# Kernel tuning notes

Hardware: AMD Instinct MI355X
Metric: run time of the kernel (lower is better)

## Reference

```python
import jax, jax.numpy as jnp
import numpy as np

N_EMBED = 8192
EMBED_DIM = 32
BETA = 0.25
EPS_NORM = 1e-12   # torch F.normalize eps
EPS_ENT = 1e-4     # get_entropy eps


def _l2norm(x):
    n = jnp.linalg.norm(x, axis=-1, keepdims=True)
    return x / jnp.maximum(n, EPS_NORM)


def setup_inputs() -> dict:
    key = jax.random.key(0)
    k1, k2 = jax.random.split(key)
    z = jax.random.normal(k1, (32, EMBED_DIM, 32, 32), dtype=jnp.float32)
    # embedding.weight.data.uniform_(-1/n_embed, 1/n_embed)
    embedding = jax.random.uniform(k2, (N_EMBED, EMBED_DIM), dtype=jnp.float32,
                                   minval=-1.0 / N_EMBED, maxval=1.0 / N_EMBED)
    return {"z": z, "embedding": embedding}


def reference(z, embedding):
    batch = z.shape[0]
    # bchw -> bhwc
    zt = jnp.transpose(z, (0, 2, 3, 1))
    # l2_norm branch: cosine distance via negative inner product
    zn = _l2norm(zt)
    z_flat = zn.reshape(-1, EMBED_DIM)            # [N, D], N = B*H*W
    ew = _l2norm(embedding)                       # [K, D]
    d = -jnp.matmul(z_flat, ew.T)                 # [N, K] distance matrix
    idx = jnp.argmin(jax.lax.stop_gradient(d), axis=1)  # [N]
    # codebook usage histogram + entropy
    cb_usage = jax.ops.segment_sum(jnp.ones_like(idx, dtype=jnp.float32), idx,
                                   num_segments=N_EMBED)
    probs = (cb_usage + EPS_ENT) / jnp.sum(cb_usage + EPS_ENT)
    cb_entropy = -jnp.sum(probs * jnp.log(probs))
    # gather + re-normalize (faithful to embedding lookup then F.normalize)
    z_q = _l2norm(embedding[idx]).reshape(zn.shape)
    sg = jax.lax.stop_gradient
    loss = (BETA * jnp.mean(jnp.sum((sg(z_q) - zn) ** 2, axis=-1))
            + jnp.mean(jnp.sum((z_q - sg(zn)) ** 2, axis=-1)))
    # straight-through estimator
    z_q_st = zn + sg(z_q - zn)
    z_q_out = jnp.transpose(z_q_st, (0, 3, 1, 2))  # bhwc -> bchw
    return z_q_out, loss, cb_entropy, idx.reshape(batch, -1)
```

## Files before the change

### kernel.cpp

```cpp
#include <hip/hip_runtime.h>
#include <math.h>

#define N_EMBED 8192
#define DIM 32
#define NQ 32768

#define QPB 512
#define NQG (NQ / QPB)
#define KSPL 8
#define KCHUNK (N_EMBED / KSPL)
#define TILE 128
#define NTILES (KCHUNK / TILE)
#define NPLANE 8
#define LSTRIDE 130

#define LOSS_OFF  1048576
#define ENT_OFF   1048577
#define IDX_OFF   1048578

typedef __attribute__((ext_vector_type(8))) _Float16 half8;
typedef __attribute__((ext_vector_type(4))) float floatx4;

__global__ __launch_bounds__(512, 4) void score_kernel(const float* __restrict__ z,
                                                       const float* __restrict__ e,
                                                       unsigned long long* __restrict__ keys16,
                                                       unsigned* __restrict__ usage,
                                                       float* __restrict__ loss_acc,
                                                       unsigned* __restrict__ done_ctr) {
    __shared__ half8 lds[2][NPLANE * LSTRIDE];

    const int t = threadIdx.x;

    if (blockIdx.x == 0) {
        for (int i = t; i < N_EMBED; i += 512)
            __hip_atomic_store(&usage[i], 0u, __ATOMIC_RELAXED, __HIP_MEMORY_SCOPE_AGENT);
        if (t == 0) {
            __hip_atomic_store(loss_acc, 0.f, __ATOMIC_RELAXED, __HIP_MEMORY_SCOPE_AGENT);
            __hip_atomic_store(done_ctr, 0u, __ATOMIC_RELAXED, __HIP_MEMORY_SCOPE_AGENT);
        }
    }

    const int lane = t & 63;
    const int w = t >> 6;
    const int quad = lane >> 4;
    const int lc = lane & 15;
    const int qg = blockIdx.x & (NQG - 1);
    const int kc = blockIdx.x >> 6;
    const int kbase = kc * KCHUNK;
    const int qbase = qg * QPB + w * 64;

    half8 ah[4], am[4];
#pragma unroll
    for (int qt = 0; qt < 4; ++qt) {
        int q = qbase + qt * 16 + lc;
        const float* zp = z + (q >> 10) * (DIM * 1024) + (q & 1023);
        float x[8];
        float ss = 0.f;
#pragma unroll
        for (int j = 0; j < 8; ++j) {
            x[j] = zp[(quad * 8 + j) * 1024];
            ss = fmaf(x[j], x[j], ss);
        }
        ss += __shfl_xor(ss, 16, 64);
        ss += __shfl_xor(ss, 32, 64);
        float inv = 1.f / fmaxf(sqrtf(ss), 1e-12f);
#pragma unroll
        for (int j = 0; j < 8; ++j) {
            float xx = x[j] * inv;
            _Float16 h = (_Float16)xx;
            _Float16 m = (_Float16)((xx - (float)h) * 4096.0f);
            ah[qt][j] = h; am[qt][j] = m;
        }
    }

    auto stage = [&](int bsel, int kt) {
        const int ci = t >> 2;
        const int part = t & 3;
        const int code = kbase + kt * TILE + ci;
        const float4* er = (const float4*)(e + code * DIM) + part * 2;
        float4 v0 = er[0], v1 = er[1];
        float x[8] = {v0.x, v0.y, v0.z, v0.w, v1.x, v1.y, v1.z, v1.w};
        float ss = 0.f;
#pragma unroll
        for (int j = 0; j < 8; ++j) ss = fmaf(x[j], x[j], ss);
        ss += __shfl_xor(ss, 1, 64);
        ss += __shfl_xor(ss, 2, 64);
        float inv = 1.f / fmaxf(sqrtf(ss), 1e-12f);
        half8 h8, m8;
#pragma unroll
        for (int j = 0; j < 8; ++j) {
            float xx = x[j] * inv;
            _Float16 h = (_Float16)xx;
            _Float16 m = (_Float16)((xx - (float)h) * 4096.0f);
            h8[j] = h; m8[j] = m;
        }
        lds[bsel][part * LSTRIDE + ci] = h8;
        lds[bsel][(4 + part) * LSTRIDE + ci] = m8;
    };

    float best[16];
    int bk[16];
#pragma unroll
    for (int i = 0; i < 16; ++i) { best[i] = -2.0f; bk[i] = 0; }

    const floatx4 z4 = {0.f, 0.f, 0.f, 0.f};

    stage(0, 0);
    __syncthreads();

    for (int kt = 0; kt < NTILES; ++kt) {
        if (kt + 1 < NTILES) stage((kt + 1) & 1, kt + 1);

        const half8* __restrict__ buf = lds[kt & 1];
#pragma unroll 2
        for (int ct = 0; ct < TILE / 16; ++ct) {
            half8 bh = buf[(0 * 4 + quad) * LSTRIDE + ct * 16 + lc];
            half8 bm = buf[(1 * 4 + quad) * LSTRIDE + ct * 16 + lc];
            const int kk = kbase + kt * TILE + ct * 16 + lc;
#pragma unroll
            for (int qt = 0; qt < 4; ++qt) {
                floatx4 a0 = __builtin_amdgcn_mfma_f32_16x16x32_f16(ah[qt], bh, z4, 0, 0, 0);
                floatx4 a1 = __builtin_amdgcn_mfma_f32_16x16x32_f16(ah[qt], bm, z4, 0, 0, 0);
                a1 = __builtin_amdgcn_mfma_f32_16x16x32_f16(am[qt], bh, a1, 0, 0, 0);
#pragma unroll
                for (int r = 0; r < 4; ++r) {
                    float d = fmaf(a1[r], 0x1p-12f, a0[r]);
                    if (d > best[qt * 4 + r]) { best[qt * 4 + r] = d; bk[qt * 4 + r] = kk; }
                }
            }
        }
        __syncthreads();
    }

#pragma unroll
    for (int i = 0; i < 16; ++i) {
        unsigned ub = __float_as_uint(best[i]);
        ub = (ub & 0x80000000u) ? ~ub : (ub | 0x80000000u);
        unsigned long long key = ((unsigned long long)ub << 32) | (unsigned)(~bk[i]);
#pragma unroll
        for (int msk = 1; msk <= 8; msk <<= 1) {
            unsigned long long o = __shfl_xor(key, msk, 64);
            key = (o > key) ? o : key;
        }
        if (lc == 0) {
            int qt = i >> 2, r = i & 3;
            int q = qbase + qt * 16 + quad * 4 + r;
            __hip_atomic_store(&keys16[kc * NQ + q], key,
                               __ATOMIC_RELAXED, __HIP_MEMORY_SCOPE_AGENT);
        }
    }
}

__global__ __launch_bounds__(256) void finalize_kernel(const float* __restrict__ z,
                                                       const float* __restrict__ e,
                                                       const unsigned long long* __restrict__ keys16,
                                                       unsigned* __restrict__ usage,
                                                       float* __restrict__ loss_acc,
                                                       unsigned* __restrict__ done_ctr,
                                                       float* __restrict__ out) {
    int n = blockIdx.x * 256 + threadIdx.x;
    int b  = n >> 10;
    int hw = n & 1023;
    const float* zb = z + b * (DIM * 1024) + hw;

    float q[DIM];
    float ss = 0.f;
#pragma unroll
    for (int d = 0; d < DIM; ++d) {
        q[d] = zb[d * 1024];
        ss = fmaf(q[d], q[d], ss);
    }
    float inv = 1.f / fmaxf(sqrtf(ss), 1e-12f);
#pragma unroll
    for (int d = 0; d < DIM; ++d) q[d] *= inv;

    unsigned long long bestkey = 0ull;
#pragma unroll
    for (int c = 0; c < KSPL; ++c) {
        unsigned long long k16 = __hip_atomic_load(&keys16[c * NQ + n],
                                                   __ATOMIC_RELAXED,
                                                   __HIP_MEMORY_SCOPE_AGENT);
        bestkey = (k16 > bestkey) ? k16 : bestkey;
    }
    int idx = (int)(~(unsigned)(bestkey & 0xFFFFFFFFull));

    atomicAdd(&usage[idx], 1u);

    float wv[DIM];
    float ss2 = 0.f;
    const float4* er = (const float4*)(e + idx * DIM);
#pragma unroll
    for (int d8 = 0; d8 < 8; ++d8) {
        float4 t4 = er[d8];
        wv[d8*4+0] = t4.x; wv[d8*4+1] = t4.y; wv[d8*4+2] = t4.z; wv[d8*4+3] = t4.w;
        ss2 += t4.x*t4.x + t4.y*t4.y + t4.z*t4.z + t4.w*t4.w;
    }
    float inv2 = 1.f / fmaxf(sqrtf(ss2), 1e-12f);

    float lsum = 0.f;
    float* outb = out + b * (DIM * 1024) + hw;
#pragma unroll
    for (int d = 0; d < DIM; ++d) {
        float zq = wv[d] * inv2;
        float diff = zq - q[d];
        lsum = fmaf(diff, diff, lsum);
        outb[d * 1024] = q[d] + (zq - q[d]);
    }
    out[IDX_OFF + n] = (float)idx;

#pragma unroll
    for (int off = 32; off > 0; off >>= 1)
        lsum += __shfl_down(lsum, off, 64);
    if ((threadIdx.x & 63) == 0)
        atomicAdd(loss_acc, lsum);

    __shared__ unsigned lastflag;
    __syncthreads();
    if (threadIdx.x == 0) {
        __threadfence();
        unsigned prev = __hip_atomic_fetch_add(done_ctr, 1u, __ATOMIC_ACQ_REL,
                                               __HIP_MEMORY_SCOPE_AGENT);
        lastflag = (prev == gridDim.x - 1) ? 1u : 0u;
    }
    __syncthreads();
    if (lastflag) {
        __shared__ double sm[256];
        int t = threadIdx.x;
        double local = 0.0;
        const float denom = 32768.8192f;
        for (int k = t; k < N_EMBED; k += 256) {
            unsigned c = __hip_atomic_load(&usage[k], __ATOMIC_RELAXED,
                                           __HIP_MEMORY_SCOPE_AGENT);
            float p = ((float)c + 1e-4f) / denom;
            local += (double)(-(p * logf(p)));
        }
        sm[t] = local;
        __syncthreads();
        for (int s = 128; s > 0; s >>= 1) {
            if (t < s) sm[t] += sm[t + s];
            __syncthreads();
        }
        if (t == 0) {
            float la = __hip_atomic_load(loss_acc, __ATOMIC_RELAXED,
                                         __HIP_MEMORY_SCOPE_AGENT);
            out[LOSS_OFF] = (float)(1.25 * (double)la / 32768.0);
            out[ENT_OFF]  = (float)sm[0];
        }
    }
}

extern "C" void kernel_launch(void* const* d_in, const int* in_sizes, int n_in,
                              void* d_out, int out_size, void* d_ws, size_t ws_size,
                              hipStream_t stream) {
    const float* z   = (const float*)d_in[0];
    const float* emb = (const float*)d_in[1];
    float* out = (float*)d_out;

    char* ws = (char*)d_ws;
    unsigned long long* keys16 = (unsigned long long*)ws;
    unsigned* usage            = (unsigned*)(ws + (2 << 20));
    float* loss_acc            = (float*)(ws + (2 << 20) + 32768);
    unsigned* done_ctr         = (unsigned*)(ws + (2 << 20) + 32768 + 4);

    score_kernel<<<NQG * KSPL, 512, 0, stream>>>(z, emb, keys16, usage,
                                                 loss_acc, done_ctr);
    finalize_kernel<<<NQ / 256, 256, 0, stream>>>(z, emb, keys16, usage,
                                                  loss_acc, done_ctr, out);
}
```

Measured before the change: 139.6 us.

## Move entropy/loss finalization into a separate single-block kernel and shrink finalize blocks

The last-block-done pattern (done counter, threadfence, acq_rel atomic) in finalize_kernel is replaced by a third single-block kernel that computes the entropy and the loss scalar. Finalize blocks drop from 256 to 128 threads, and each block now does one loss atomic after an LDS reduction instead of one per wave. This removes the per-block fence and counter atomic and the serialized tail work inside the last block, at the cost of an extra kernel launch.

```diff
diff --git a/kernel.cpp b/kernel.cpp
--- a/kernel.cpp
+++ b/kernel.cpp
@@ -25,8 +25,7 @@
                                                        const float* __restrict__ e,
                                                        unsigned long long* __restrict__ keys16,
                                                        unsigned* __restrict__ usage,
-                                                       float* __restrict__ loss_acc,
-                                                       unsigned* __restrict__ done_ctr) {
+                                                       float* __restrict__ loss_acc) {
     __shared__ half8 lds[2][NPLANE * LSTRIDE];
 
     const int t = threadIdx.x;
@@ -34,10 +33,8 @@
     if (blockIdx.x == 0) {
         for (int i = t; i < N_EMBED; i += 512)
             __hip_atomic_store(&usage[i], 0u, __ATOMIC_RELAXED, __HIP_MEMORY_SCOPE_AGENT);
-        if (t == 0) {
+        if (t == 0)
             __hip_atomic_store(loss_acc, 0.f, __ATOMIC_RELAXED, __HIP_MEMORY_SCOPE_AGENT);
-            __hip_atomic_store(done_ctr, 0u, __ATOMIC_RELAXED, __HIP_MEMORY_SCOPE_AGENT);
-        }
     }
 
     const int lane = t & 63;
@@ -151,14 +148,13 @@
     }
 }
 
-__global__ __launch_bounds__(256) void finalize_kernel(const float* __restrict__ z,
+__global__ __launch_bounds__(128) void finalize_kernel(const float* __restrict__ z,
                                                        const float* __restrict__ e,
                                                        const unsigned long long* __restrict__ keys16,
                                                        unsigned* __restrict__ usage,
                                                        float* __restrict__ loss_acc,
-                                                       unsigned* __restrict__ done_ctr,
                                                        float* __restrict__ out) {
-    int n = blockIdx.x * 256 + threadIdx.x;
+    int n = blockIdx.x * 128 + threadIdx.x;
     int b  = n >> 10;
     int hw = n & 1023;
     const float* zb = z + b * (DIM * 1024) + hw;
@@ -211,41 +207,37 @@
 #pragma unroll
     for (int off = 32; off > 0; off >>= 1)
         lsum += __shfl_down(lsum, off, 64);
-    if ((threadIdx.x & 63) == 0)
-        atomicAdd(loss_acc, lsum);
-
-    __shared__ unsigned lastflag;
+    __shared__ float wsum[2];
+    if ((threadIdx.x & 63) == 0) wsum[threadIdx.x >> 6] = lsum;
     __syncthreads();
-    if (threadIdx.x == 0) {
-        __threadfence();
-        unsigned prev = __hip_atomic_fetch_add(done_ctr, 1u, __ATOMIC_ACQ_REL,
-                                               __HIP_MEMORY_SCOPE_AGENT);
-        lastflag = (prev == gridDim.x - 1) ? 1u : 0u;
-    }
+    if (threadIdx.x == 0)
+        atomicAdd(loss_acc, wsum[0] + wsum[1]);
+}
+
+__global__ __launch_bounds__(256) void scalar_kernel(const unsigned* __restrict__ usage,
+                                                     const float* __restrict__ loss_acc,
+                                                     float* __restrict__ out) {
+    __shared__ double sm[256];
+    int t = threadIdx.x;
+    double local = 0.0;
+    const float denom = 32768.8192f;
+    for (int k = t; k < N_EMBED; k += 256) {
+        unsigned c = __hip_atomic_load(&usage[k], __ATOMIC_RELAXED,
+                                       __HIP_MEMORY_SCOPE_AGENT);
+        float p = ((float)c + 1e-4f) / denom;
+        local += (double)(-(p * logf(p)));
+    }
+    sm[t] = local;
     __syncthreads();
-    if (lastflag) {
-        __shared__ double sm[256];
-        int t = threadIdx.x;
-        double local = 0.0;
-        const float denom = 32768.8192f;
-        for (int k = t; k < N_EMBED; k += 256) {
-            unsigned c = __hip_atomic_load(&usage[k], __ATOMIC_RELAXED,
-                                           __HIP_MEMORY_SCOPE_AGENT);
-            float p = ((float)c + 1e-4f) / denom;
-            local += (double)(-(p * logf(p)));
-        }
-        sm[t] = local;
+    for (int s = 128; s > 0; s >>= 1) {
+        if (t < s) sm[t] += sm[t + s];
         __syncthreads();
-        for (int s = 128; s > 0; s >>= 1) {
-            if (t < s) sm[t] += sm[t + s];
-            __syncthreads();
-        }
-        if (t == 0) {
-            float la = __hip_atomic_load(loss_acc, __ATOMIC_RELAXED,
-                                         __HIP_MEMORY_SCOPE_AGENT);
-            out[LOSS_OFF] = (float)(1.25 * (double)la / 32768.0);
-            out[ENT_OFF]  = (float)sm[0];
-        }
+    }
+    if (t == 0) {
+        float la = __hip_atomic_load(loss_acc, __ATOMIC_RELAXED,
+                                     __HIP_MEMORY_SCOPE_AGENT);
+        out[LOSS_OFF] = (float)(1.25 * (double)la / 32768.0);
+        out[ENT_OFF]  = (float)sm[0];
     }
 }
 
@@ -260,10 +252,9 @@
     unsigned long long* keys16 = (unsigned long long*)ws;
     unsigned* usage            = (unsigned*)(ws + (2 << 20));
     float* loss_acc            = (float*)(ws + (2 << 20) + 32768);
-    unsigned* done_ctr         = (unsigned*)(ws + (2 << 20) + 32768 + 4);
-
-    score_kernel<<<NQG * KSPL, 512, 0, stream>>>(z, emb, keys16, usage,
-                                                 loss_acc, done_ctr);
-    finalize_kernel<<<NQ / 256, 256, 0, stream>>>(z, emb, keys16, usage,
-                                                  loss_acc, done_ctr, out);
-}
+
+    score_kernel<<<NQG * KSPL, 512, 0, stream>>>(z, emb, keys16, usage, loss_acc);
+    finalize_kernel<<<NQ / 128, 128, 0, stream>>>(z, emb, keys16, usage,
+                                                  loss_acc, out);
+    scalar_kernel<<<1, 256, 0, stream>>>(usage, loss_acc, out);
+}
```

Measured after the change: 133.1 us. -4.7%, faster.
